# Kernel tuning notes

Measured on AMD Instinct MI355X. Metric: run time of the kernel, lower is better.

The kernel has to match this reference:

```python
import jax, jax.numpy as jnp
import numpy as np

N, E, F, L, G, T = 50000, 800000, 128, 3, 256, 10


def _lin_init(key, shape, fan_in):
    s = 1.0 / np.sqrt(fan_in)
    return jax.random.uniform(key, shape, jnp.float32, -s, s)


def setup_inputs() -> dict:
    key = jax.random.key(0)
    ks = jax.random.split(key, 10)
    x = jax.random.normal(ks[0], (N, F), jnp.float32)
    edge_index = jax.random.randint(ks[1], (2, E), 0, N, jnp.int64)
    batch = jnp.sort(jax.random.randint(ks[2], (N,), 0, G, jnp.int64))
    Wl = _lin_init(ks[3], (L, F, F), F)   # lin_l weight per layer
    bl = _lin_init(ks[4], (L, F), F)      # lin_l bias per layer
    Wr = _lin_init(ks[5], (L, F, F), F)   # lin_r weight per layer (no bias)
    W1 = _lin_init(ks[6], (F, L * F), L * F)
    b1 = _lin_init(ks[7], (F,), L * F)
    W2 = _lin_init(ks[8], (T, F), F)
    b2 = _lin_init(ks[9], (T,), F)
    return {"x": x, "edge_index": edge_index, "batch": batch, "Wl": Wl,
            "bl": bl, "Wr": Wr, "W1": W1, "b1": b1, "W2": W2, "b2": b2}


def reference(x, edge_index, batch, Wl, bl, Wr, W1, b1, W2, b2):
    src, dst = edge_index[0], edge_index[1]
    n = x.shape[0]
    # in-degree for mean aggregation (zero-degree nodes -> 0, like scatter_mean)
    deg = jax.ops.segment_sum(jnp.ones_like(src, dtype=x.dtype), dst, num_segments=n)
    inv_deg = jnp.where(deg > 0, 1.0 / deg, 0.0)[:, None]
    h = x
    feats = []
    for i in range(L):
        # SAGEConv (aggr='mean'): out = lin_l(mean_j x_j) + lin_r(x_i)
        agg = jax.ops.segment_sum(h[src], dst, num_segments=n) * inv_deg
        h = agg @ Wl[i].T + bl[i] + h @ Wr[i].T
        feats.append(h)
    hc = jnp.concatenate(feats, axis=1)            # [N, L*F]
    pooled = jax.ops.segment_max(hc, batch, num_segments=G)  # global_max_pool
    z = jax.nn.relu(pooled @ W1.T + b1)
    return z @ W2.T + b2                            # [G, T]
```

## Files before the change

### kernel.cpp

```cpp
#include <hip/hip_runtime.h>
#include <math.h>


typedef __attribute__((ext_vector_type(8))) short short8v;
typedef __attribute__((ext_vector_type(4))) float f32x4;

__device__ __forceinline__ unsigned short bf_hi_bits(float f) {
    union { float f; unsigned u; } c; c.f = f;
    return (unsigned short)(c.u >> 16);
}
__device__ __forceinline__ float bf_to_f(unsigned short h) {
    union { unsigned u; float f; } c; c.u = ((unsigned)h) << 16;
    return c.f;
}

__global__ void zero_ints(int* __restrict__ p, int n) {
    int i = blockIdx.x * 256 + threadIdx.x;
    if (i < n) p[i] = 0;
}

__global__ void count_deg(const int* __restrict__ dst, int* __restrict__ deg, int E) {
    int e = blockIdx.x * 256 + threadIdx.x;
    if (e < E) atomicAdd(&deg[dst[e]], 1);
}

__global__ void make_inv_deg(const int* __restrict__ deg, float* __restrict__ inv_deg, int n) {
    int i = blockIdx.x * 256 + threadIdx.x;
    if (i < n) {
        int d = deg[i];
        inv_deg[i] = d > 0 ? 1.0f / (float)d : 0.0f;
    }
}

__global__ __launch_bounds__(256) void block_reduce_deg(const int* __restrict__ deg,
                                                        int* __restrict__ bsum, int n) {
    __shared__ int s[256];
    int t = threadIdx.x;
    int i = blockIdx.x * 256 + t;
    s[t] = (i < n) ? deg[i] : 0;
    __syncthreads();
#pragma unroll
    for (int off = 128; off > 0; off >>= 1) {
        if (t < off) s[t] += s[t + off];
        __syncthreads();
    }
    if (t == 0) bsum[blockIdx.x] = s[0];
}

__global__ __launch_bounds__(256) void scan_bsums(const int* __restrict__ bsum,
                                                  int* __restrict__ boff,
                                                  int* __restrict__ row_ptr, int nb, int n) {
    __shared__ int s[256];
    int t = threadIdx.x;
    int v = (t < nb) ? bsum[t] : 0;
    s[t] = v;
    __syncthreads();
#pragma unroll
    for (int off = 1; off < 256; off <<= 1) {
        int u = (t >= off) ? s[t - off] : 0;
        __syncthreads();
        s[t] += u;
        __syncthreads();
    }
    if (t < nb) boff[t] = s[t] - v;
    if (t == 255) row_ptr[n] = s[255];
}

__global__ __launch_bounds__(256) void scan_fill(const int* __restrict__ deg,
                                                 const int* __restrict__ boff,
                                                 int* __restrict__ row_ptr,
                                                 int* __restrict__ fill_pos, int n) {
    __shared__ int s[256];
    int t = threadIdx.x;
    int i = blockIdx.x * 256 + t;
    int v = (i < n) ? deg[i] : 0;
    s[t] = v;
    __syncthreads();
#pragma unroll
    for (int off = 1; off < 256; off <<= 1) {
        int u = (t >= off) ? s[t - off] : 0;
        __syncthreads();
        s[t] += u;
        __syncthreads();
    }
    if (i < n) {
        int ex = boff[blockIdx.x] + s[t] - v;
        row_ptr[i] = ex;
        fill_pos[i] = ex;
    }
}

__global__ void fill_csr(const int* __restrict__ src, const int* __restrict__ dst,
                         int* __restrict__ fill_pos, int* __restrict__ csr_src, int E) {
    int e = blockIdx.x * 256 + threadIdx.x;
    if (e < E) {
        int d = dst[e];
        int pos = atomicAdd(&fill_pos[d], 1);
        csr_src[pos] = src[e];
    }
}

__global__ __launch_bounds__(256) void aggregate(const float* __restrict__ h, int hstride,
                                                 const int* __restrict__ row_ptr,
                                                 const int* __restrict__ csr_src,
                                                 const float* __restrict__ inv_deg,
                                                 float* __restrict__ agg, int n) {
    int node = blockIdx.x * 4 + (threadIdx.x >> 6);
    if (node >= n) return;
    int lane = threadIdx.x & 63;
    int half = lane >> 5;
    int li = lane & 31;
    int j0 = row_ptr[node], j1 = row_ptr[node + 1];
    float ax0 = 0.f, ay0 = 0.f, az0 = 0.f, aw0 = 0.f;
    float ax1 = 0.f, ay1 = 0.f, az1 = 0.f, aw1 = 0.f;
    int j = j0 + half;
    for (; j + 2 < j1; j += 4) {
        int s0 = csr_src[j];
        int s1 = csr_src[j + 2];
        float4 v0 = *(const float4*)(h + (size_t)s0 * hstride + li * 4);
        float4 v1 = *(const float4*)(h + (size_t)s1 * hstride + li * 4);
        ax0 += v0.x; ay0 += v0.y; az0 += v0.z; aw0 += v0.w;
        ax1 += v1.x; ay1 += v1.y; az1 += v1.z; aw1 += v1.w;
    }
    if (j < j1) {
        int s0 = csr_src[j];
        float4 v0 = *(const float4*)(h + (size_t)s0 * hstride + li * 4);
        ax0 += v0.x; ay0 += v0.y; az0 += v0.z; aw0 += v0.w;
    }
    float ax = ax0 + ax1, ay = ay0 + ay1, az = az0 + az1, aw = aw0 + aw1;
    ax += __shfl_xor(ax, 32);
    ay += __shfl_xor(ay, 32);
    az += __shfl_xor(az, 32);
    aw += __shfl_xor(aw, 32);
    if (half == 0) {
        float w = inv_deg[node];
        float4 o = {ax * w, ay * w, az * w, aw * w};
        *(float4*)(agg + (size_t)node * 128 + li * 4) = o;
    }
}

__global__ void prep_wext(const float* __restrict__ Wl, const float* __restrict__ Wr,
                          unsigned short* __restrict__ wext) {
    int idx = blockIdx.x * 256 + threadIdx.x;
    if (idx >= 36864) return;
    int layer = idx / 12288;
    int rem = idx - layer * 12288;
    int s = rem / 2048;
    int rem2 = rem - s * 2048;
    int c = rem2 >> 4;
    int kc = (rem2 & 15) * 8;
    const float* W = (s < 3 ? Wl : Wr) + (size_t)layer * 16384 + c * 128 + kc;
    bool lo = (s % 3) == 1;
    unsigned short* o = wext + (((size_t)layer * 6 + s) * 16384) + c * 128 + kc;
#pragma unroll
    for (int i = 0; i < 8; ++i) {
        float f = W[i];
        unsigned short hb = bf_hi_bits(f);
        if (lo) hb = bf_hi_bits(f - bf_to_f(hb));
        o[i] = hb;
    }
}

__global__ __launch_bounds__(256, 2) void gemm_mfma(const float* __restrict__ A1,
                                                    const float* __restrict__ A2, int stride2,
                                                    const unsigned short* __restrict__ wext,
                                                    const float* __restrict__ bl,
                                                    float* __restrict__ out, int n) {
    __shared__ unsigned short Ald[16384];
    __shared__ unsigned short Wld[16384];

    const int tid = threadIdx.x;
    const int row0 = blockIdx.x * 128;
    const int wid = tid >> 6;
    const int lane = tid & 63;
    const int lrow = lane & 15;
    const int lk = lane >> 4;
    const int RowB = (wid >> 1) * 64;
    const int ColB = (wid & 1) * 64;

    const f32x4 zf = {0.f, 0.f, 0.f, 0.f};
    f32x4 acc[4][4];
#pragma unroll
    for (int i = 0; i < 4; ++i)
#pragma unroll
        for (int j = 0; j < 4; ++j) acc[i][j] = zf;

    const int sr = tid >> 1;
    const int sh = tid & 1;
    int grow = row0 + sr;
    if (grow > n - 1) grow = n - 1;
    const float* a1p = A1 + (size_t)grow * 128 + sh * 64;
    const float* a2p = A2 + (size_t)grow * stride2 + sh * 64;
    const int sbyte = sr * 256 + sh * 128;
    const int sswz = (sr & 7) << 4;

    const int needA[6] = {1, 0, 1, 1, 0, 1};
    const int srcA[6] = {0, 0, 0, 1, 1, 1};
    const int loA[6] = {0, 0, 1, 0, 0, 1};

    for (int s = 0; s < 6; ++s) {
        const unsigned short* wsrc = wext + s * 16384 + sr * 128 + sh * 64;
#pragma unroll
        for (int i = 0; i < 8; ++i) {
            short8v w = *(const short8v*)(wsrc + i * 8);
            *(short8v*)((char*)Wld + sbyte + ((i * 16) ^ sswz)) = w;
        }
        if (needA[s]) {
            const float* ap = srcA[s] ? a2p : a1p;
            const bool lo = loA[s] != 0;
#pragma unroll
            for (int i = 0; i < 8; ++i) {
                float4 f0 = *(const float4*)(ap + i * 8);
                float4 f1 = *(const float4*)(ap + i * 8 + 4);
                float ff[8] = {f0.x, f0.y, f0.z, f0.w, f1.x, f1.y, f1.z, f1.w};
                short8v v;
#pragma unroll
                for (int j = 0; j < 8; ++j) {
                    unsigned short hb = bf_hi_bits(ff[j]);
                    if (lo) hb = bf_hi_bits(ff[j] - bf_to_f(hb));
                    v[j] = (short)hb;
                }
                *(short8v*)((char*)Ald + sbyte + ((i * 16) ^ sswz)) = v;
            }
        }
        __syncthreads();
#pragma unroll
        for (int ks = 0; ks < 4; ++ks) {
            short8v af[4], bfr[4];
#pragma unroll
            for (int mr = 0; mr < 4; ++mr) {
                int r = RowB + mr * 16 + lrow;
                int byte = (r * 256 + ks * 64 + lk * 16) ^ ((r & 7) << 4);
                af[mr] = *(const short8v*)((const char*)Ald + byte);
            }
#pragma unroll
            for (int nr = 0; nr < 4; ++nr) {
                int c = ColB + nr * 16 + lrow;
                int byte = (c * 256 + ks * 64 + lk * 16) ^ ((c & 7) << 4);
                bfr[nr] = *(const short8v*)((const char*)Wld + byte);
            }
#pragma unroll
            for (int mr = 0; mr < 4; ++mr)
#pragma unroll
                for (int nr = 0; nr < 4; ++nr)
                    acc[mr][nr] = __builtin_amdgcn_mfma_f32_16x16x32_bf16(
                        af[mr], bfr[nr], acc[mr][nr], 0, 0, 0);
        }
        __syncthreads();
    }

#pragma unroll
    for (int nr = 0; nr < 4; ++nr) {
        int col = ColB + nr * 16 + lrow;
        float bias = bl[col];
#pragma unroll
        for (int mr = 0; mr < 4; ++mr) {
            int rbase = row0 + RowB + mr * 16 + lk * 4;
#pragma unroll
            for (int r = 0; r < 4; ++r) {
                int row = rbase + r;
                if (row < n) out[(size_t)row * 384 + col] = acc[mr][nr][r] + bias;
            }
        }
    }
}

__global__ void find_starts(const int* __restrict__ batch, int* __restrict__ start, int n, int G) {
    int i = blockIdx.x * 256 + threadIdx.x;
    if (i >= n) return;
    int b = batch[i];
    if (i == 0) {
        for (int g = 0; g <= b; ++g) start[g] = 0;
    } else {
        int pb = batch[i - 1];
        for (int g = pb + 1; g <= b; ++g) start[g] = i;
    }
    if (i == n - 1) {
        for (int g = b + 1; g <= G; ++g) start[g] = n;
    }
}

__global__ __launch_bounds__(384) void pool_max(const float* __restrict__ hc,
                                                const int* __restrict__ start,
                                                float* __restrict__ pooled, int G) {
    int g = blockIdx.x;
    int f = threadIdx.x;
    int s = start[g], e = start[g + 1];
    float m = -INFINITY;
    for (int node = s; node < e; ++node) m = fmaxf(m, hc[(size_t)node * 384 + f]);
    pooled[(size_t)g * 384 + f] = m;
}

__global__ __launch_bounds__(128) void mlp_head(const float* __restrict__ pooled,
                                                const float* __restrict__ W1,
                                                const float* __restrict__ b1,
                                                const float* __restrict__ W2,
                                                const float* __restrict__ b2,
                                                float* __restrict__ out) {
    __shared__ float p[384];
    __shared__ float z[128];
    int g = blockIdx.x, t = threadIdx.x;
    for (int k = t; k < 384; k += 128) p[k] = pooled[(size_t)g * 384 + k];
    __syncthreads();
    float acc = b1[t];
#pragma unroll 4
    for (int k = 0; k < 384; k += 4) {
        float4 w = *(const float4*)(W1 + (size_t)t * 384 + k);
        acc += p[k] * w.x + p[k + 1] * w.y + p[k + 2] * w.z + p[k + 3] * w.w;
    }
    z[t] = fmaxf(acc, 0.f);
    __syncthreads();
    if (t < 10) {
        float a2 = b2[t];
#pragma unroll 8
        for (int k = 0; k < 128; ++k) a2 += z[k] * W2[t * 128 + k];
        out[g * 10 + t] = a2;
    }
}

extern "C" void kernel_launch(void* const* d_in, const int* in_sizes, int n_in,
                              void* d_out, int out_size, void* d_ws, size_t ws_size,
                              hipStream_t stream) {
    const float* x = (const float*)d_in[0];
    const int* edge = (const int*)d_in[1];
    const int* batch = (const int*)d_in[2];
    const float* Wl = (const float*)d_in[3];
    const float* bl = (const float*)d_in[4];
    const float* Wr = (const float*)d_in[5];
    const float* W1 = (const float*)d_in[6];
    const float* b1 = (const float*)d_in[7];
    const float* W2 = (const float*)d_in[8];
    const float* b2 = (const float*)d_in[9];
    float* out = (float*)d_out;

    const int F = 128, G = 256;
    const int N = in_sizes[0] / F;
    const int E = in_sizes[1] / 2;
    const int NB = (N + 255) / 256;

    const int* src = edge;
    const int* dst = edge + E;

    char* p = (char*)d_ws;
    auto alloc = [&](size_t bytes) {
        char* r = p;
        p += (bytes + 15) & ~(size_t)15;
        return r;
    };
    float* hc = (float*)alloc((size_t)N * 384 * 4);
    float* agg = (float*)alloc((size_t)N * 128 * 4);
    float* inv = (float*)alloc((size_t)N * 4);
    float* pooled = (float*)alloc((size_t)G * 384 * 4);
    int* deg = (int*)alloc((size_t)N * 4);
    int* row_ptr = (int*)alloc((size_t)(N + 1) * 4);
    int* fillp = (int*)alloc((size_t)N * 4);
    int* csr = (int*)alloc((size_t)E * 4);
    int* start = (int*)alloc((size_t)(G + 1) * 4);
    unsigned short* wext = (unsigned short*)alloc((size_t)3 * 6 * 16384 * 2);
    int* bsum = (int*)alloc((size_t)NB * 4);
    int* boff = (int*)alloc((size_t)NB * 4);

    zero_ints<<<NB, 256, 0, stream>>>(deg, N);
    count_deg<<<(E + 255) / 256, 256, 0, stream>>>(dst, deg, E);
    make_inv_deg<<<NB, 256, 0, stream>>>(deg, inv, N);
    block_reduce_deg<<<NB, 256, 0, stream>>>(deg, bsum, N);
    scan_bsums<<<1, 256, 0, stream>>>(bsum, boff, row_ptr, NB, N);
    scan_fill<<<NB, 256, 0, stream>>>(deg, boff, row_ptr, fillp, N);
    fill_csr<<<(E + 255) / 256, 256, 0, stream>>>(src, dst, fillp, csr, E);
    prep_wext<<<144, 256, 0, stream>>>(Wl, Wr, wext);

    for (int l = 0; l < 3; ++l) {
        const float* hin = (l == 0) ? x : (hc + (size_t)(l - 1) * 128);
        int hstride = (l == 0) ? 128 : 384;
        aggregate<<<(N + 3) / 4, 256, 0, stream>>>(hin, hstride, row_ptr, csr, inv, agg, N);
        gemm_mfma<<<(N + 127) / 128, 256, 0, stream>>>(
            agg, hin, hstride, wext + (size_t)l * 6 * 16384, bl + (size_t)l * F,
            hc + (size_t)l * 128, N);
    }

    find_starts<<<NB, 256, 0, stream>>>(batch, start, N, G);
    pool_max<<<G, 384, 0, stream>>>(hc, start, pooled, G);
    mlp_head<<<G, 128, 0, stream>>>(pooled, W1, b1, W2, b2, out);
}
```

Measured before the change: 525.1 us.

## Gather neighbor features from a bf16 shadow copy during aggregation

Adds a bf16 copy of the node features. The input x is converted up front, and the GEMM epilogue writes the bf16 copy alongside the fp32 output. The edge gather in aggregation now reads these 2-byte values, halving the bytes fetched per edge, and accumulates in fp32. It also folds the inverse-degree computation into the block reduction kernel, removing one launch, and unrolls the GEMM stage loop. The cost is an extra conversion pass, extra bf16 stores, and bf16 rounding of the aggregated inputs, which may affect accuracy against the fp32 reference.

Result: faster. 500.2 us (-4.7%).

```diff
diff --git a/kernel.cpp b/kernel.cpp
--- a/kernel.cpp
+++ b/kernel.cpp
@@ -13,6 +13,12 @@
     union { unsigned u; float f; } c; c.u = ((unsigned)h) << 16;
     return c.f;
 }
+__device__ __forceinline__ unsigned short f2bf_rne(float f) {
+    union { float f; unsigned u; } c; c.f = f;
+    unsigned u = c.u;
+    u += 0x7FFF + ((u >> 16) & 1);
+    return (unsigned short)(u >> 16);
+}
 
 __global__ void zero_ints(int* __restrict__ p, int n) {
     int i = blockIdx.x * 256 + threadIdx.x;
@@ -24,20 +30,18 @@
     if (e < E) atomicAdd(&deg[dst[e]], 1);
 }
 
-__global__ void make_inv_deg(const int* __restrict__ deg, float* __restrict__ inv_deg, int n) {
-    int i = blockIdx.x * 256 + threadIdx.x;
-    if (i < n) {
-        int d = deg[i];
-        inv_deg[i] = d > 0 ? 1.0f / (float)d : 0.0f;
-    }
-}
-
 __global__ __launch_bounds__(256) void block_reduce_deg(const int* __restrict__ deg,
-                                                        int* __restrict__ bsum, int n) {
+                                                        int* __restrict__ bsum,
+                                                        float* __restrict__ inv_deg, int n) {
     __shared__ int s[256];
     int t = threadIdx.x;
     int i = blockIdx.x * 256 + t;
-    s[t] = (i < n) ? deg[i] : 0;
+    int d = 0;
+    if (i < n) {
+        d = deg[i];
+        inv_deg[i] = d > 0 ? 1.0f / (float)d : 0.0f;
+    }
+    s[t] = d;
     __syncthreads();
 #pragma unroll
     for (int off = 128; off > 0; off >>= 1) {
@@ -100,34 +104,44 @@
     }
 }
 
-__global__ __launch_bounds__(256) void aggregate(const float* __restrict__ h, int hstride,
-                                                 const int* __restrict__ row_ptr,
-                                                 const int* __restrict__ csr_src,
-                                                 const float* __restrict__ inv_deg,
-                                                 float* __restrict__ agg, int n) {
+__global__ void f32_to_bf16(const float* __restrict__ in, unsigned short* __restrict__ out,
+                            int n4) {
+    int i = blockIdx.x * 256 + threadIdx.x;
+    if (i < n4) {
+        float4 v = *(const float4*)(in + (size_t)i * 4);
+        ushort4 o = {f2bf_rne(v.x), f2bf_rne(v.y), f2bf_rne(v.z), f2bf_rne(v.w)};
+        *(ushort4*)(out + (size_t)i * 4) = o;
+    }
+}
+
+__global__ __launch_bounds__(256) void aggregate_bf(const unsigned short* __restrict__ hb,
+                                                    const int* __restrict__ row_ptr,
+                                                    const int* __restrict__ csr_src,
+                                                    const float* __restrict__ inv_deg,
+                                                    float* __restrict__ agg, int n) {
     int node = blockIdx.x * 4 + (threadIdx.x >> 6);
     if (node >= n) return;
     int lane = threadIdx.x & 63;
     int half = lane >> 5;
     int li = lane & 31;
     int j0 = row_ptr[node], j1 = row_ptr[node + 1];
-    float ax0 = 0.f, ay0 = 0.f, az0 = 0.f, aw0 = 0.f;
-    float ax1 = 0.f, ay1 = 0.f, az1 = 0.f, aw1 = 0.f;
+    float a0 = 0.f, a1 = 0.f, a2 = 0.f, a3 = 0.f;
+    float b0 = 0.f, b1 = 0.f, b2 = 0.f, b3 = 0.f;
     int j = j0 + half;
     for (; j + 2 < j1; j += 4) {
         int s0 = csr_src[j];
         int s1 = csr_src[j + 2];
-        float4 v0 = *(const float4*)(h + (size_t)s0 * hstride + li * 4);
-        float4 v1 = *(const float4*)(h + (size_t)s1 * hstride + li * 4);
-        ax0 += v0.x; ay0 += v0.y; az0 += v0.z; aw0 += v0.w;
-        ax1 += v1.x; ay1 += v1.y; az1 += v1.z; aw1 += v1.w;
+        ushort4 v0 = *(const ushort4*)(hb + (size_t)s0 * 128 + li * 4);
+        ushort4 v1 = *(const ushort4*)(hb + (size_t)s1 * 128 + li * 4);
+        a0 += bf_to_f(v0.x); a1 += bf_to_f(v0.y); a2 += bf_to_f(v0.z); a3 += bf_to_f(v0.w);
+        b0 += bf_to_f(v1.x); b1 += bf_to_f(v1.y); b2 += bf_to_f(v1.z); b3 += bf_to_f(v1.w);
     }
     if (j < j1) {
         int s0 = csr_src[j];
-        float4 v0 = *(const float4*)(h + (size_t)s0 * hstride + li * 4);
-        ax0 += v0.x; ay0 += v0.y; az0 += v0.z; aw0 += v0.w;
-    }
-    float ax = ax0 + ax1, ay = ay0 + ay1, az = az0 + az1, aw = aw0 + aw1;
+        ushort4 v0 = *(const ushort4*)(hb + (size_t)s0 * 128 + li * 4);
+        a0 += bf_to_f(v0.x); a1 += bf_to_f(v0.y); a2 += bf_to_f(v0.z); a3 += bf_to_f(v0.w);
+    }
+    float ax = a0 + b0, ay = a1 + b1, az = a2 + b2, aw = a3 + b3;
     ax += __shfl_xor(ax, 32);
     ay += __shfl_xor(ay, 32);
     az += __shfl_xor(az, 32);
@@ -165,7 +179,8 @@
                                                     const float* __restrict__ A2, int stride2,
                                                     const unsigned short* __restrict__ wext,
                                                     const float* __restrict__ bl,
-                                                    float* __restrict__ out, int n) {
+                                                    float* __restrict__ out,
+                                                    unsigned short* __restrict__ outb, int n) {
     __shared__ unsigned short Ald[16384];
     __shared__ unsigned short Wld[16384];
 
@@ -198,6 +213,7 @@
     const int srcA[6] = {0, 0, 0, 1, 1, 1};
     const int loA[6] = {0, 0, 1, 0, 0, 1};
 
+#pragma unroll
     for (int s = 0; s < 6; ++s) {
         const unsigned short* wsrc = wext + s * 16384 + sr * 128 + sh * 64;
 #pragma unroll
@@ -259,7 +275,11 @@
 #pragma unroll
             for (int r = 0; r < 4; ++r) {
                 int row = rbase + r;
-                if (row < n) out[(size_t)row * 384 + col] = acc[mr][nr][r] + bias;
+                if (row < n) {
+                    float v = acc[mr][nr][r] + bias;
+                    out[(size_t)row * 384 + col] = v;
+                    if (outb) outb[(size_t)row * 128 + col] = f2bf_rne(v);
+                }
             }
         }
     }
@@ -359,23 +379,24 @@
     unsigned short* wext = (unsigned short*)alloc((size_t)3 * 6 * 16384 * 2);
     int* bsum = (int*)alloc((size_t)NB * 4);
     int* boff = (int*)alloc((size_t)NB * 4);
+    unsigned short* hb = (unsigned short*)alloc((size_t)N * 128 * 2);
 
     zero_ints<<<NB, 256, 0, stream>>>(deg, N);
     count_deg<<<(E + 255) / 256, 256, 0, stream>>>(dst, deg, E);
-    make_inv_deg<<<NB, 256, 0, stream>>>(deg, inv, N);
-    block_reduce_deg<<<NB, 256, 0, stream>>>(deg, bsum, N);
+    block_reduce_deg<<<NB, 256, 0, stream>>>(deg, bsum, inv, N);
     scan_bsums<<<1, 256, 0, stream>>>(bsum, boff, row_ptr, NB, N);
     scan_fill<<<NB, 256, 0, stream>>>(deg, boff, row_ptr, fillp, N);
     fill_csr<<<(E + 255) / 256, 256, 0, stream>>>(src, dst, fillp, csr, E);
     prep_wext<<<144, 256, 0, stream>>>(Wl, Wr, wext);
+    f32_to_bf16<<<(N * 32 + 255) / 256, 256, 0, stream>>>(x, hb, N * 32);
 
     for (int l = 0; l < 3; ++l) {
         const float* hin = (l == 0) ? x : (hc + (size_t)(l - 1) * 128);
         int hstride = (l == 0) ? 128 : 384;
-        aggregate<<<(N + 3) / 4, 256, 0, stream>>>(hin, hstride, row_ptr, csr, inv, agg, N);
+        aggregate_bf<<<(N + 3) / 4, 256, 0, stream>>>(hb, row_ptr, csr, inv, agg, N);
         gemm_mfma<<<(N + 127) / 128, 256, 0, stream>>>(
             agg, hin, hstride, wext + (size_t)l * 6 * 16384, bl + (size_t)l * F,
-            hc + (size_t)l * 128, N);
+            hc + (size_t)l * 128, (l < 2) ? hb : (unsigned short*)nullptr, N);
     }
 
     find_starts<<<NB, 256, 0, stream>>>(batch, start, N, G);
```
